# Optimization experiments

Measured on AMD Instinct MI355X. Metric: run time of the kernel, lower is better.

## Reference

```python
import jax, jax.numpy as jnp
import numpy as np

ALPHA, GAMMA = 0.25, 2.0
COST_CLASS, COST_BBOX, COST_GIOU = 2.0, 5.0, 2.0
EPS = 1e-8


def box_cxcywh_to_xyxy(b):
    cx, cy, w, h = b[..., 0], b[..., 1], b[..., 2], b[..., 3]
    return jnp.stack([cx - 0.5 * w, cy - 0.5 * h, cx + 0.5 * w, cy + 0.5 * h], axis=-1)


def generalized_box_iou(boxes1, boxes2):
    # boxes1: [N,4] xyxy, boxes2: [M,4] xyxy -> [N,M] GIoU
    area1 = (boxes1[:, 2] - boxes1[:, 0]) * (boxes1[:, 3] - boxes1[:, 1])
    area2 = (boxes2[:, 2] - boxes2[:, 0]) * (boxes2[:, 3] - boxes2[:, 1])
    lt = jnp.maximum(boxes1[:, None, :2], boxes2[None, :, :2])   # [N,M,2]
    rb = jnp.minimum(boxes1[:, None, 2:], boxes2[None, :, 2:])   # [N,M,2]
    wh = jnp.clip(rb - lt, 0.0)
    inter = wh[..., 0] * wh[..., 1]
    union = area1[:, None] + area2[None, :] - inter
    iou = inter / union
    # smallest enclosing box
    lt_c = jnp.minimum(boxes1[:, None, :2], boxes2[None, :, :2])
    rb_c = jnp.maximum(boxes1[:, None, 2:], boxes2[None, :, 2:])
    wh_c = jnp.clip(rb_c - lt_c, 0.0)
    area_c = wh_c[..., 0] * wh_c[..., 1]
    return iou - (area_c - union) / area_c


def setup_inputs() -> dict:
    key = jax.random.key(0)
    k1, k2, k3, k4 = jax.random.split(key, 4)
    BS, NQ, NC, NT = 16, 900, 91, 960
    pred_logits = jax.random.normal(k1, (BS, NQ, NC), dtype=jnp.float32)
    pred_boxes = jax.random.uniform(k2, (BS, NQ, 4), dtype=jnp.float32)
    tgt_ids = jax.random.randint(k3, (NT,), 0, NC, dtype=jnp.int64)
    tgt_bbox = jax.random.uniform(k4, (NT, 4), dtype=jnp.float32)
    return {"pred_logits": pred_logits, "pred_boxes": pred_boxes,
            "tgt_ids": tgt_ids, "tgt_bbox": tgt_bbox}


def reference(pred_logits, pred_boxes, tgt_ids, tgt_bbox):
    bs, nq, _ = pred_logits.shape
    out_prob = jax.nn.sigmoid(pred_logits.reshape(bs * nq, -1))      # [BN, C]
    out_bbox = pred_boxes.reshape(bs * nq, 4)                         # [BN, 4]
    # focal-style classification cost, gathered at target class ids
    neg_cost = (1.0 - ALPHA) * out_prob ** GAMMA * (-jnp.log(1.0 - out_prob + EPS))
    pos_cost = ALPHA * (1.0 - out_prob) ** GAMMA * (-jnp.log(out_prob + EPS))
    cost_class = pos_cost[:, tgt_ids] - neg_cost[:, tgt_ids]          # [BN, NT]
    # pairwise L1 distance between boxes (cxcywh space), like torch.cdist(p=1)
    cost_bbox = jnp.sum(jnp.abs(out_bbox[:, None, :] - tgt_bbox[None, :, :]), axis=-1)
    cost_giou = -generalized_box_iou(box_cxcywh_to_xyxy(out_bbox),
                                     box_cxcywh_to_xyxy(tgt_bbox))    # [BN, NT]
    C = COST_BBOX * cost_bbox + COST_CLASS * cost_class + COST_GIOU * cost_giou
    return C.reshape(bs, nq, -1)
```

## Files before the change

### kernel.cpp

```cpp
#include <hip/hip_runtime.h>
#include <math.h>


#define ALPHA_F   0.25f
#define COST_CLS  2.0f
#define COST_BBOX 5.0f
#define COST_GIOU 2.0f
#define EPS_F     1e-8f

constexpr int THREADS = 256;

typedef float vfloat4 __attribute__((ext_vector_type(4)));

template<int NC, int NT>
__global__ __launch_bounds__(THREADS) void matcher_kernel_s(
    const float* __restrict__ logits,
    const float* __restrict__ boxes,
    const int*   __restrict__ tids,
    const float* __restrict__ tboxes,
    float*       __restrict__ out)
{
    constexpr int ROWS = 2;
    constexpr int JPT  = 4;
    constexpr int NJT  = NT / JPT;
    constexpr int NTAB = ROWS * NC;
    constexpr int CSTR = 3;

    __shared__ float s_cls[NC * CSTR];

    const int tid  = threadIdx.x;
    const int row0 = blockIdx.x * ROWS;
    const bool active = tid < NJT;

    float x = 0.0f;
    if (tid < NTAB)
        x = logits[(size_t)row0 * NC + tid];

    float4 tb[JPT];
    int ic[JPT] = {0, 0, 0, 0};
    if (active) {
        const int4 tv = reinterpret_cast<const int4*>(tids)[tid];
        ic[0] = tv.x; ic[1] = tv.y; ic[2] = tv.z; ic[3] = tv.w;
        #pragma unroll
        for (int k = 0; k < JPT; ++k)
            tb[k] = reinterpret_cast<const float4*>(tboxes)[tid * JPT + k];
    } else {
        #pragma unroll
        for (int k = 0; k < JPT; ++k) tb[k] = make_float4(0.f, 0.f, 0.f, 0.f);
    }

    if (tid < NTAB) {
        const float p  = 1.0f / (1.0f + __expf(-x));
        const float om = 1.0f - p;
        const float neg = (1.0f - ALPHA_F) * p * p * (-__logf(om + EPS_F));
        const float pos = ALPHA_F * om * om        * (-__logf(p  + EPS_F));
        const int r = (tid >= NC) ? 1 : 0;
        const int c = tid - (r ? NC : 0);
        s_cls[c * CSTR + r] = COST_CLS * (pos - neg) + COST_GIOU;
    }
    __syncthreads();

    if (!active) return;

    float cc0[JPT], cc1[JPT];
    #pragma unroll
    for (int k = 0; k < JPT; ++k) {
        const float* cp = s_cls + ic[k] * CSTR;
        cc0[k] = cp[0];
        cc1[k] = cp[1];
    }

    float* __restrict__ optr = out + (size_t)row0 * NT + tid * JPT;
    #pragma unroll
    for (int r = 0; r < ROWS; ++r) {
        const float4 pb = reinterpret_cast<const float4*>(boxes)[row0 + r];
        const float px0 = pb.x - 0.5f * pb.z, py0 = pb.y - 0.5f * pb.w;
        const float px1 = pb.x + 0.5f * pb.z, py1 = pb.y + 0.5f * pb.w;
        const float parea = pb.z * pb.w;

        float rv[JPT];
        #pragma unroll
        for (int k = 0; k < JPT; ++k) {
            const float4 t = tb[k];
            const float hw = 0.5f * t.z, hh = 0.5f * t.w;
            const float tx0 = t.x - hw, tx1 = t.x + hw;
            const float ty0 = t.y - hh, ty1 = t.y + hh;
            const float tarea = t.z * t.w;
            const float l1 = (fabsf(pb.x - t.x) + fabsf(pb.y - t.y))
                           + (fabsf(pb.z - t.z) + fabsf(pb.w - t.w));
            const float iwr = fminf(px1, tx1) - fmaxf(px0, tx0);
            const float ihr = fminf(py1, ty1) - fmaxf(py0, ty0);
            const float inter = fmaxf(iwr, 0.0f) * fmaxf(ihr, 0.0f);
            const float uni = (parea + tarea) - inter;
            const float cw = (pb.z + t.z) - iwr;
            const float ch = (pb.w + t.w) - ihr;
            const float carea = cw * ch;
            const float num  = fmaf(inter, carea, uni * uni);
            const float rcpd = __builtin_amdgcn_rcpf(uni * carea);
            const float ctab = (r == 0) ? cc0[k] : cc1[k];
            const float base = fmaf(COST_BBOX, l1, ctab);
            rv[k] = fmaf(-2.0f * num, rcpd, base);
        }
        vfloat4 v;
        v.x = rv[0]; v.y = rv[1]; v.z = rv[2]; v.w = rv[3];
        __builtin_nontemporal_store(v, reinterpret_cast<vfloat4*>(optr));
        optr += NT;
    }
}

constexpr int GROWS = 8;
__global__ __launch_bounds__(THREADS) void matcher_kernel_g(
    const float* __restrict__ logits, const float* __restrict__ boxes,
    const int* __restrict__ tids, const float* __restrict__ tboxes,
    float* __restrict__ out, int BN, int NC, int NT)
{
    extern __shared__ float s_cls_g[];
    const int tid  = threadIdx.x;
    const int row0 = blockIdx.x * GROWS;
    const int nrows = (BN - row0 < GROWS) ? (BN - row0) : GROWS;

    for (int t = tid; t < nrows * NC; t += THREADS) {
        const int r = t / NC, c = t - r * NC;
        const float x  = logits[(size_t)(row0 + r) * NC + c];
        const float p  = 1.0f / (1.0f + expf(-x));
        const float om = 1.0f - p;
        const float neg = (1.0f - ALPHA_F) * p * p * (-logf(om + EPS_F));
        const float pos = ALPHA_F * om * om        * (-logf(p + EPS_F));
        s_cls_g[r * NC + c] = pos - neg;
    }
    __syncthreads();

    for (int r = 0; r < nrows; ++r) {
        const int row = row0 + r;
        const float4 pb = reinterpret_cast<const float4*>(boxes)[row];
        const float px0 = pb.x - 0.5f * pb.z, py0 = pb.y - 0.5f * pb.w;
        const float px1 = pb.x + 0.5f * pb.z, py1 = pb.y + 0.5f * pb.w;
        const float parea = pb.z * pb.w;
        for (int j = tid; j < NT; j += THREADS) {
            const float4 b = reinterpret_cast<const float4*>(tboxes)[j];
            const float bx0 = b.x - 0.5f * b.z, by0 = b.y - 0.5f * b.w;
            const float bx1 = b.x + 0.5f * b.z, by1 = b.y + 0.5f * b.w;
            const float l1 = fabsf(pb.x - b.x) + fabsf(pb.y - b.y)
                           + fabsf(pb.z - b.z) + fabsf(pb.w - b.w);
            const float iw = fmaxf(fminf(px1, bx1) - fmaxf(px0, bx0), 0.0f);
            const float ih = fmaxf(fminf(py1, by1) - fmaxf(py0, by0), 0.0f);
            const float inter = iw * ih;
            const float uni = parea + b.z * b.w - inter;
            const float iou = inter / uni;
            const float cw = fmaxf(px1, bx1) - fminf(px0, bx0);
            const float ch = fmaxf(py1, by1) - fminf(py0, by0);
            const float carea = cw * ch;
            const float giou = iou - (carea - uni) / carea;
            const float ccls = s_cls_g[r * NC + tids[j]];
            out[(size_t)row * NT + j] = COST_BBOX * l1 + COST_CLS * ccls - COST_GIOU * giou;
        }
        __syncthreads();
    }
}

extern "C" void kernel_launch(void* const* d_in, const int* in_sizes, int n_in,
                              void* d_out, int out_size, void* d_ws, size_t ws_size,
                              hipStream_t stream) {
    const float* logits = (const float*)d_in[0];
    const float* boxes  = (const float*)d_in[1];
    const int*   tids   = (const int*)d_in[2];
    const float* tboxes = (const float*)d_in[3];
    float* out = (float*)d_out;

    const int BN = in_sizes[1] / 4;
    const int NC = in_sizes[0] / BN;
    const int NT = in_sizes[2];

    if (NC == 91 && NT == 960 && BN % 2 == 0) {
        const int grid = BN / 2;
        matcher_kernel_s<91, 960><<<grid, THREADS, 0, stream>>>(
            logits, boxes, tids, tboxes, out);
    } else {
        const int grid = (BN + GROWS - 1) / GROWS;
        const size_t shmem = (size_t)GROWS * NC * sizeof(float);
        matcher_kernel_g<<<grid, THREADS, shmem, stream>>>(
            logits, boxes, tids, tboxes, out, BN, NC, NT);
    }
}
```

Baseline: 20.96 us.

## Split focal class-cost table into separate kernel, drop shared-memory barrier

Precomputes the per-row focal classification cost table in a separate kernel, writing it to a padded workspace buffer. The matcher kernel then gathers the table values from global memory, so it no longer needs shared memory or __syncthreads. This removes the barrier and the transcendental math from the critical path of the main kernel. In exchange it adds a second launch and a round trip of the table through global memory. The old fused kernel is kept as a fallback when the workspace is too small.

```diff
diff --git a/kernel.cpp b/kernel.cpp
--- a/kernel.cpp
+++ b/kernel.cpp
@@ -12,9 +12,31 @@
 
 typedef float vfloat4 __attribute__((ext_vector_type(4)));
 
+__device__ __forceinline__ float focal_entry(float x) {
+    const float p  = 1.0f / (1.0f + __expf(-x));
+    const float om = 1.0f - p;
+    const float neg = (1.0f - ALPHA_F) * p * p * (-__logf(om + EPS_F));
+    const float pos = ALPHA_F * om * om        * (-__logf(p  + EPS_F));
+    return COST_CLS * (pos - neg) + COST_GIOU;
+}
+
+template<int NC, int NCP>
+__global__ __launch_bounds__(THREADS) void focal_table_kernel(
+    const float* __restrict__ logits,
+    float*       __restrict__ tab,
+    int total)
+{
+    const int idx = blockIdx.x * THREADS + threadIdx.x;
+    if (idx >= total) return;
+    const int row = idx / NC;
+    const int c   = idx - row * NC;
+    const float x = __builtin_nontemporal_load(logits + idx);
+    tab[(size_t)row * NCP + c] = focal_entry(x);
+}
+
 template<int NC, int NT>
-__global__ __launch_bounds__(THREADS) void matcher_kernel_s(
-    const float* __restrict__ logits,
+__global__ __launch_bounds__(THREADS) void matcher_k2(
+    const float* __restrict__ tab,
     const float* __restrict__ boxes,
     const int*   __restrict__ tids,
     const float* __restrict__ tboxes,
@@ -23,52 +45,24 @@
     constexpr int ROWS = 2;
     constexpr int JPT  = 4;
     constexpr int NJT  = NT / JPT;
-    constexpr int NTAB = ROWS * NC;
-    constexpr int CSTR = 3;
-
-    __shared__ float s_cls[NC * CSTR];
+    constexpr int NCP  = 96;
 
     const int tid  = threadIdx.x;
     const int row0 = blockIdx.x * ROWS;
-    const bool active = tid < NJT;
-
-    float x = 0.0f;
-    if (tid < NTAB)
-        x = logits[(size_t)row0 * NC + tid];
+    if (tid >= NJT) return;
+
+    const int4 tv = reinterpret_cast<const int4*>(tids)[tid];
+    const int ic[JPT] = {tv.x, tv.y, tv.z, tv.w};
+    const float* __restrict__ t0 = tab + (size_t)row0 * NCP;
+    const float* __restrict__ t1 = t0 + NCP;
+    float cc0[JPT], cc1[JPT];
+    #pragma unroll
+    for (int k = 0; k < JPT; ++k) { cc0[k] = t0[ic[k]]; cc1[k] = t1[ic[k]]; }
 
     float4 tb[JPT];
-    int ic[JPT] = {0, 0, 0, 0};
-    if (active) {
-        const int4 tv = reinterpret_cast<const int4*>(tids)[tid];
-        ic[0] = tv.x; ic[1] = tv.y; ic[2] = tv.z; ic[3] = tv.w;
-        #pragma unroll
-        for (int k = 0; k < JPT; ++k)
-            tb[k] = reinterpret_cast<const float4*>(tboxes)[tid * JPT + k];
-    } else {
-        #pragma unroll
-        for (int k = 0; k < JPT; ++k) tb[k] = make_float4(0.f, 0.f, 0.f, 0.f);
-    }
-
-    if (tid < NTAB) {
-        const float p  = 1.0f / (1.0f + __expf(-x));
-        const float om = 1.0f - p;
-        const float neg = (1.0f - ALPHA_F) * p * p * (-__logf(om + EPS_F));
-        const float pos = ALPHA_F * om * om        * (-__logf(p  + EPS_F));
-        const int r = (tid >= NC) ? 1 : 0;
-        const int c = tid - (r ? NC : 0);
-        s_cls[c * CSTR + r] = COST_CLS * (pos - neg) + COST_GIOU;
-    }
-    __syncthreads();
-
-    if (!active) return;
-
-    float cc0[JPT], cc1[JPT];
-    #pragma unroll
-    for (int k = 0; k < JPT; ++k) {
-        const float* cp = s_cls + ic[k] * CSTR;
-        cc0[k] = cp[0];
-        cc1[k] = cp[1];
-    }
+    #pragma unroll
+    for (int k = 0; k < JPT; ++k)
+        tb[k] = reinterpret_cast<const float4*>(tboxes)[tid * JPT + k];
 
     float* __restrict__ optr = out + (size_t)row0 * NT + tid * JPT;
     #pragma unroll
@@ -108,6 +102,95 @@
     }
 }
 
+template<int NC, int NT>
+__global__ __launch_bounds__(THREADS) void matcher_kernel_s(
+    const float* __restrict__ logits, const float* __restrict__ boxes,
+    const int* __restrict__ tids, const float* __restrict__ tboxes,
+    float* __restrict__ out)
+{
+    constexpr int ROWS = 2;
+    constexpr int JPT  = 4;
+    constexpr int NJT  = NT / JPT;
+    constexpr int NTAB = ROWS * NC;
+    constexpr int CSTR = 3;
+
+    __shared__ float s_cls[NC * CSTR];
+
+    const int tid  = threadIdx.x;
+    const int row0 = blockIdx.x * ROWS;
+    const bool active = tid < NJT;
+
+    float x = 0.0f;
+    if (tid < NTAB) x = logits[(size_t)row0 * NC + tid];
+
+    float4 tb[JPT];
+    int ic[JPT] = {0, 0, 0, 0};
+    if (active) {
+        const int4 tv = reinterpret_cast<const int4*>(tids)[tid];
+        ic[0] = tv.x; ic[1] = tv.y; ic[2] = tv.z; ic[3] = tv.w;
+        #pragma unroll
+        for (int k = 0; k < JPT; ++k)
+            tb[k] = reinterpret_cast<const float4*>(tboxes)[tid * JPT + k];
+    } else {
+        #pragma unroll
+        for (int k = 0; k < JPT; ++k) tb[k] = make_float4(0.f, 0.f, 0.f, 0.f);
+    }
+
+    if (tid < NTAB) {
+        const int r = (tid >= NC) ? 1 : 0;
+        const int c = tid - (r ? NC : 0);
+        s_cls[c * CSTR + r] = focal_entry(x);
+    }
+    __syncthreads();
+
+    if (!active) return;
+
+    float cc0[JPT], cc1[JPT];
+    #pragma unroll
+    for (int k = 0; k < JPT; ++k) {
+        const float* cp = s_cls + ic[k] * CSTR;
+        cc0[k] = cp[0];
+        cc1[k] = cp[1];
+    }
+
+    float* __restrict__ optr = out + (size_t)row0 * NT + tid * JPT;
+    #pragma unroll
+    for (int r = 0; r < ROWS; ++r) {
+        const float4 pb = reinterpret_cast<const float4*>(boxes)[row0 + r];
+        const float px0 = pb.x - 0.5f * pb.z, py0 = pb.y - 0.5f * pb.w;
+        const float px1 = pb.x + 0.5f * pb.z, py1 = pb.y + 0.5f * pb.w;
+        const float parea = pb.z * pb.w;
+
+        float rv[JPT];
+        #pragma unroll
+        for (int k = 0; k < JPT; ++k) {
+            const float4 t = tb[k];
+            const float hw = 0.5f * t.z, hh = 0.5f * t.w;
+            const float tx0 = t.x - hw, tx1 = t.x + hw;
+            const float ty0 = t.y - hh, ty1 = t.y + hh;
+            const float tarea = t.z * t.w;
+            const float l1 = (fabsf(pb.x - t.x) + fabsf(pb.y - t.y))
+                           + (fabsf(pb.z - t.z) + fabsf(pb.w - t.w));
+            const float iwr = fminf(px1, tx1) - fmaxf(px0, tx0);
+            const float ihr = fminf(py1, ty1) - fmaxf(py0, ty0);
+            const float inter = fmaxf(iwr, 0.0f) * fmaxf(ihr, 0.0f);
+            const float uni = (parea + tarea) - inter;
+            const float cw = (pb.z + t.z) - iwr;
+            const float ch = (pb.w + t.w) - ihr;
+            const float carea = cw * ch;
+            const float num  = fmaf(inter, carea, uni * uni);
+            const float rcpd = __builtin_amdgcn_rcpf(uni * carea);
+            const float ctab = (r == 0) ? cc0[k] : cc1[k];
+            const float base = fmaf(COST_BBOX, l1, ctab);
+            rv[k] = fmaf(-2.0f * num, rcpd, base);
+        }
+        vfloat4 v;
+        v.x = rv[0]; v.y = rv[1]; v.z = rv[2]; v.w = rv[3];
+        __builtin_nontemporal_store(v, reinterpret_cast<vfloat4*>(optr));
+        optr += NT;
+    }
+}
+
 constexpr int GROWS = 8;
 __global__ __launch_bounds__(THREADS) void matcher_kernel_g(
     const float* __restrict__ logits, const float* __restrict__ boxes,
@@ -121,7 +204,7 @@
 
     for (int t = tid; t < nrows * NC; t += THREADS) {
         const int r = t / NC, c = t - r * NC;
-        const float x  = logits[(size_t)(row0 + r) * NC + c];
+        const float x = logits[(size_t)(row0 + r) * NC + c];
         const float p  = 1.0f / (1.0f + expf(-x));
         const float om = 1.0f - p;
         const float neg = (1.0f - ALPHA_F) * p * p * (-logf(om + EPS_F));
@@ -172,9 +255,18 @@
     const int NT = in_sizes[2];
 
     if (NC == 91 && NT == 960 && BN % 2 == 0) {
-        const int grid = BN / 2;
-        matcher_kernel_s<91, 960><<<grid, THREADS, 0, stream>>>(
-            logits, boxes, tids, tboxes, out);
+        const size_t tab_bytes = (size_t)BN * 96 * sizeof(float);
+        if (ws_size >= tab_bytes) {
+            float* tab = (float*)d_ws;
+            const int total = BN * NC;
+            const int g1 = (total + THREADS - 1) / THREADS;
+            focal_table_kernel<91, 96><<<g1, THREADS, 0, stream>>>(logits, tab, total);
+            matcher_k2<91, 960><<<BN / 2, THREADS, 0, stream>>>(
+                tab, boxes, tids, tboxes, out);
+        } else {
+            matcher_kernel_s<91, 960><<<BN / 2, THREADS, 0, stream>>>(
+                logits, boxes, tids, tboxes, out);
+        }
     } else {
         const int grid = (BN + GROWS - 1) / GROWS;
         const size_t shmem = (size_t)GROWS * NC * sizeof(float);
```

Measured after the change: 30.09 us. 1.44x slower.
